# Optimization experiments

Measured on AMD Instinct MI355X. Metric: run time of the kernel, lower is better.

The kernel has to match this reference:

```python
import jax, jax.numpy as jnp
import numpy as np

N_NODES = 32
GAT_OUT = 64
LSTM_H = 128
N_CLS = 4
NEG_SLOPE = 0.2


def setup_inputs() -> dict:
    key = jax.random.key(0)
    ks = jax.random.split(key, 12)
    B, T, E = 32, 512, 96
    F, H = GAT_OUT, LSTM_H
    s = 0.05
    return {
        "x_seq": jax.random.normal(ks[0], (B, T, N_NODES), jnp.float32),
        "edge_index": jax.random.randint(ks[1], (2, E), 0, N_NODES, jnp.int32),
        # GATConv params (heads=1): lin weight [in=1, F], attention vectors [F], bias [F]
        "w_gat": jax.random.normal(ks[2], (1, F), jnp.float32) * s,
        "att_src": jax.random.normal(ks[3], (F,), jnp.float32) * s,
        "att_dst": jax.random.normal(ks[4], (F,), jnp.float32) * s,
        "b_gat": jnp.zeros((F,), jnp.float32),
        # LSTM params, torch gate order (i, f, g, o)
        "W_ih": jax.random.normal(ks[5], (N_NODES * F, 4 * H), jnp.float32) * s,
        "W_hh": jax.random.normal(ks[6], (H, 4 * H), jnp.float32) * s,
        "b_ih": jnp.zeros((4 * H,), jnp.float32),
        "b_hh": jnp.zeros((4 * H,), jnp.float32),
        # classifier
        "W_fc": jax.random.normal(ks[7], (H, N_CLS), jnp.float32) * s,
        "b_fc": jnp.zeros((N_CLS,), jnp.float32),
    }


def _forward(x_seq, edge_index, w_gat, att_src, att_dst, b_gat,
             W_ih, W_hh, b_ih, b_hh, W_fc, b_fc):
    B, T, N = x_seq.shape
    F = w_gat.shape[1]
    H = W_hh.shape[0]

    # --- GAT over all (B,T) steps at once (PyG GATConv, heads=1, self-loops) ---
    loops = jnp.arange(N, dtype=edge_index.dtype)
    src = jnp.concatenate([edge_index[0], loops])  # [Et]
    dst = jnp.concatenate([edge_index[1], loops])  # [Et]
    Et = src.shape[0]

    h = x_seq[..., None] * w_gat            # [B,T,N,F] (in_channels=1 linear)
    a_s = h @ att_src                        # [B,T,N]
    a_d = h @ att_dst                        # [B,T,N]
    e = a_s[..., src] + a_d[..., dst]        # [B,T,Et]
    e = jnp.where(e > 0, e, NEG_SLOPE * e)   # LeakyReLU(0.2)

    # segment softmax over destination node, batched over B*T
    e2 = jnp.moveaxis(e, -1, 0).reshape(Et, B * T)
    m = jax.ops.segment_max(e2, dst, num_segments=N)        # [N,B*T]
    ex = jnp.exp(e2 - m[dst])
    z = jax.ops.segment_sum(ex, dst, num_segments=N)        # [N,B*T]
    alpha = ex / z[dst]                                      # [Et,B*T]
    alpha = jnp.moveaxis(alpha.reshape(Et, B, T), 0, -1)     # [B,T,Et]

    msg = alpha[..., None] * h[:, :, src, :]                 # [B,T,Et,F]
    onehot = (dst[:, None] == jnp.arange(N)).astype(h.dtype)  # [Et,N]
    out = jnp.einsum('btef,en->btnf', msg, onehot) + b_gat    # [B,T,N,F]

    seq = out.reshape(B, T, N * F)           # [B,T,2048]

    # --- single-layer LSTM (batch_first), torch gate order i,f,g,o ---
    xw = seq @ W_ih + (b_ih + b_hh)          # [B,T,4H]

    def step(carry, xw_t):
        hs, cs = carry
        g = xw_t + hs @ W_hh                 # [B,4H]
        i, f, gg, o = jnp.split(g, 4, axis=-1)
        cs = jax.nn.sigmoid(f) * cs + jax.nn.sigmoid(i) * jnp.tanh(gg)
        hs = jax.nn.sigmoid(o) * jnp.tanh(cs)
        return (hs, cs), None

    h0 = jnp.zeros((B, H), seq.dtype)
    (h_last, _), _ = jax.lax.scan(step, (h0, h0), jnp.moveaxis(xw, 1, 0))

    return h_last @ W_fc + b_fc              # [B,num_classes]


def reference(x_seq, edge_index, w_gat, att_src, att_dst, b_gat,
              W_ih, W_hh, b_ih, b_hh, W_fc, b_fc):
    return _forward(x_seq, edge_index, w_gat, att_src, att_dst, b_gat,
                    W_ih, W_hh, b_ih, b_hh, W_fc, b_fc)
```

## Files before the change

### kernel.cpp

```cpp
#include <hip/hip_runtime.h>
#include <hip/hip_fp16.h>

#define NN 32
#define FF 64
#define HH 128
#define G4 512
#define BB 32
#define TT 512
#define ET 128
#define NPOS (BB*TT)
#define POSB 32

__device__ __forceinline__ float frcp(float x) { return __builtin_amdgcn_rcpf(x); }

__global__ __launch_bounds__(512) void prep_kernel(const float* __restrict__ w_gat,
                                                   const float* __restrict__ b_gat,
                                                   const float* __restrict__ W_ih,
                                                   const float* __restrict__ W_hh,
                                                   float* __restrict__ W_eff,
                                                   float* __restrict__ biasp,
                                                   float* __restrict__ Wt) {
  int j = threadIdx.x;
  int n = blockIdx.x;
  float accw = 0.f, accb = 0.f;
#pragma unroll 8
  for (int f = 0; f < FF; ++f) {
    float wv = W_ih[(n * FF + f) * G4 + j];
    accw = fmaf(w_gat[f], wv, accw);
    accb = fmaf(b_gat[f], wv, accb);
  }
  W_eff[n * G4 + j] = accw;
  biasp[n * G4 + j] = accb;
  __half* Wt16 = (__half*)Wt;
  int g0 = (n * G4 + j) * 4;
#pragma unroll
  for (int q = 0; q < 4; ++q) {
    int E = g0 + q;
    int tl = E >> 7, idx = E & 127;
    int r = tl >> 2, kq = tl & 3;
    int P = idx >> 3;
    int g = (idx >> 1) & 3;
    int e = idx & 1;
    int k = kq * 32 + 2 * P + e;
    Wt16[E] = __float2half(W_hh[k * G4 + g * 128 + r]);
  }
}

__global__ __launch_bounds__(256) void gatxw_kernel(const float* __restrict__ x_seq,
                                                    const int* __restrict__ ei,
                                                    const float* __restrict__ w_gat,
                                                    const float* __restrict__ att_src,
                                                    const float* __restrict__ att_dst,
                                                    const float* __restrict__ b_ih,
                                                    const float* __restrict__ b_hh,
                                                    const float* __restrict__ W_eff,
                                                    const float* __restrict__ biasp,
                                                    float* __restrict__ xw) {
  __shared__ int srt[ET];
  __shared__ int offs[NN + 1];
  __shared__ int cnt[NN];
  __shared__ float xs[POSB * NN];
  __shared__ float sl[POSB * NN];
  __shared__ float scal_sh[2];
  int tid = threadIdx.x;
  int posbase = blockIdx.x * POSB;
  float we0[NN], we1[NN];
#pragma unroll
  for (int nn = 0; nn < NN; ++nn) {
    we0[nn] = W_eff[nn * G4 + tid];
    we1[nn] = W_eff[nn * G4 + 256 + tid];
  }
  float b0 = b_ih[tid] + b_hh[tid];
  float b1 = b_ih[256 + tid] + b_hh[256 + tid];
#pragma unroll 8
  for (int n = 0; n < NN; ++n) {
    b0 += biasp[n * G4 + tid];
    b1 += biasp[n * G4 + 256 + tid];
  }
  if (tid < NN) cnt[tid] = 0;
  __syncthreads();
  int es = 0, ed = 0, tk = 0;
  if (tid < ET) {
    if (tid < 96) { es = ei[tid]; ed = ei[96 + tid]; }
    else { es = tid - 96; ed = tid - 96; }
    tk = atomicAdd(&cnt[ed], 1);
  }
  __syncthreads();
  if (tid == 0) {
    offs[0] = 0;
    for (int n = 0; n < NN; ++n) offs[n + 1] = offs[n] + cnt[n];
  }
  if (tid == 1) {
    float cs = 0.f, cd = 0.f;
    for (int f = 0; f < FF; ++f) {
      cs = fmaf(w_gat[f], att_src[f], cs);
      cd = fmaf(w_gat[f], att_dst[f], cd);
    }
    scal_sh[0] = cs;
    scal_sh[1] = cd;
  }
  __syncthreads();
  if (tid < ET) srt[offs[ed] + tk] = es;
#pragma unroll
  for (int c = 0; c < POSB * NN / 256; ++c)
    xs[c * 256 + tid] = x_seq[posbase * NN + c * 256 + tid];
  __syncthreads();
  float cs = scal_sh[0], cd = scal_sh[1];
  int n = tid & 31;
  int e0 = offs[n], e1 = offs[n + 1];
#pragma unroll
  for (int pb = 0; pb < POSB / 8; ++pb) {
    int p = pb * 8 + (tid >> 5);
    int base = p * 32;
    float xn = xs[base + n];
    float cdxn = cd * xn;
    float m = -3.0e38f;
    for (int e = e0; e < e1; ++e) {
      float ev = fmaf(cs, xs[base + srt[e]], cdxn);
      ev = ev > 0.f ? ev : 0.2f * ev;
      m = fmaxf(m, ev);
    }
    float z = 0.f, sa = 0.f;
    for (int e = e0; e < e1; ++e) {
      float xsv = xs[base + srt[e]];
      float ev = fmaf(cs, xsv, cdxn);
      ev = ev > 0.f ? ev : 0.2f * ev;
      float ex = __expf(ev - m);
      z += ex;
      sa = fmaf(ex, xsv, sa);
    }
    sl[base + n] = sa * frcp(z);
  }
  __syncthreads();
#pragma unroll 4
  for (int pp = 0; pp < POSB; ++pp) {
    const float4* sp = (const float4*)&sl[pp * 32];
    float a0 = b0, a1 = b1;
#pragma unroll
    for (int q = 0; q < 8; ++q) {
      float4 sv = sp[q];
      a0 = fmaf(sv.x, we0[4 * q], a0);
      a0 = fmaf(sv.y, we0[4 * q + 1], a0);
      a0 = fmaf(sv.z, we0[4 * q + 2], a0);
      a0 = fmaf(sv.w, we0[4 * q + 3], a0);
      a1 = fmaf(sv.x, we1[4 * q], a1);
      a1 = fmaf(sv.y, we1[4 * q + 1], a1);
      a1 = fmaf(sv.z, we1[4 * q + 2], a1);
      a1 = fmaf(sv.w, we1[4 * q + 3], a1);
    }
    size_t row = (size_t)(posbase + pp) * G4;
    xw[row + tid] = a0;
    xw[row + 256 + tid] = a1;
  }
}


#define D2F(HJ, W0, W1, W2, W3) \
  "v_dot2_f32_f16 v216, v" HJ ", v" W0 ", 0\n\t" \
  "v_dot2_f32_f16 v217, v" HJ ", v" W1 ", 0\n\t" \
  "v_dot2_f32_f16 v218, v" HJ ", v" W2 ", 0\n\t" \
  "v_dot2_f32_f16 v219, v" HJ ", v" W3 ", 0\n\t"

#define D2A(HJ, W0, W1, W2, W3) \
  "v_dot2_f32_f16 v216, v" HJ ", v" W0 ", v216\n\t" \
  "v_dot2_f32_f16 v217, v" HJ ", v" W1 ", v217\n\t" \
  "v_dot2_f32_f16 v218, v" HJ ", v" W2 ", v218\n\t" \
  "v_dot2_f32_f16 v219, v" HJ ", v" W3 ", v219\n\t"

#define PHASE(XSLOT, RD, WR) \
  "ds_read_b128 v[32:35], " RD "\n\t" \
  "ds_read_b128 v[36:39], " RD " offset:16\n\t" \
  "ds_read_b128 v[40:43], " RD " offset:32\n\t" \
  "ds_read_b128 v[44:47], " RD " offset:48\n\t" \
  "s_waitcnt lgkmcnt(3)\n\t" \
  D2F("32", "64", "65", "66", "67") \
  D2A("33", "68", "69", "70", "71") \
  D2A("34", "72", "73", "74", "75") \
  D2A("35", "76", "77", "78", "79") \
  "s_waitcnt lgkmcnt(2)\n\t" \
  D2A("36", "80", "81", "82", "83") \
  D2A("37", "84", "85", "86", "87") \
  D2A("38", "88", "89", "90", "91") \
  D2A("39", "92", "93", "94", "95") \
  "s_waitcnt lgkmcnt(1)\n\t" \
  D2A("40", "96", "97", "98", "99") \
  D2A("41", "100", "101", "102", "103") \
  D2A("42", "104", "105", "106", "107") \
  D2A("43", "108", "109", "110", "111") \
  "s_waitcnt lgkmcnt(0)\n\t" \
  D2A("44", "112", "113", "114", "115") \
  D2A("45", "116", "117", "118", "119") \
  D2A("46", "120", "121", "122", "123") \
  D2A("47", "124", "125", "126", "127") \
  "v_add_f32_dpp v216, v216, v216 quad_perm:[1,0,3,2] row_mask:0xf bank_mask:0xf\n\t" \
  "v_add_f32_dpp v217, v217, v217 quad_perm:[1,0,3,2] row_mask:0xf bank_mask:0xf\n\t" \
  "v_add_f32_dpp v218, v218, v218 quad_perm:[1,0,3,2] row_mask:0xf bank_mask:0xf\n\t" \
  "v_add_f32_dpp v219, v219, v219 quad_perm:[1,0,3,2] row_mask:0xf bank_mask:0xf\n\t" \
  "v_add_f32_dpp v216, v216, v216 quad_perm:[2,3,0,1] row_mask:0xf bank_mask:0xf\n\t" \
  "v_add_f32_dpp v217, v217, v217 quad_perm:[2,3,0,1] row_mask:0xf bank_mask:0xf\n\t" \
  "v_add_f32_dpp v218, v218, v218 quad_perm:[2,3,0,1] row_mask:0xf bank_mask:0xf\n\t" \
  "v_add_f32_dpp v219, v219, v219 quad_perm:[2,3,0,1] row_mask:0xf bank_mask:0xf\n\t" \
  "v_cndmask_b32 v208, v216, v217, s[22:23]\n\t" \
  "v_cndmask_b32 v209, v218, v219, s[22:23]\n\t" \
  "v_cndmask_b32 v208, v208, v209, s[24:25]\n\t" \
  "s_waitcnt vmcnt(3)\n\t" \
  "v_mov_b32 v215, " XSLOT "\n\t" \
  "global_load_dword " XSLOT ", v194, %[xwb]\n\t" \
  "v_add_u32 v194, 0x800, v194\n\t" \
  "v_add_f32 v208, v208, v215\n\t" \
  "v_mul_f32 v209, v200, v208\n\t" \
  "v_exp_f32 v209, v209\n\t" \
  "s_nop 0\n\t" \
  "v_add_f32 v209, 1.0, v209\n\t" \
  "v_rcp_f32 v209, v209\n\t" \
  "s_nop 0\n\t" \
  "v_fma_f32 v210, v201, v209, v202\n\t" \
  "s_nop 1\n\t" \
  "v_add_f32_dpp v211, v210, v203 quad_perm:[0,0,0,0] row_mask:0xf bank_mask:0xf\n\t" \
  "v_add_f32_dpp v212, v210, v203 quad_perm:[1,1,1,1] row_mask:0xf bank_mask:0xf\n\t" \
  "v_add_f32_dpp v213, v210, v203 quad_perm:[2,2,2,2] row_mask:0xf bank_mask:0xf\n\t" \
  "v_add_f32_dpp v214, v210, v203 quad_perm:[3,3,3,3] row_mask:0xf bank_mask:0xf\n\t" \
  "v_mul_f32 v211, v211, v213\n\t" \
  "v_fma_f32 v199, v212, v199, v211\n\t" \
  "v_mul_f32 v209, 0x4038aa3b, v199\n\t" \
  "v_exp_f32 v209, v209\n\t" \
  "s_nop 0\n\t" \
  "v_add_f32 v209, 1.0, v209\n\t" \
  "v_rcp_f32 v209, v209\n\t" \
  "s_nop 0\n\t" \
  "v_fma_f32 v209, -2.0, v209, 1.0\n\t" \
  "v_mul_f32 v209, v214, v209\n\t" \
  "v_cvt_f16_f32 v209, v209\n\t" \
  "ds_write_b16 " WR ", v209\n\t" \
  "s_waitcnt lgkmcnt(0)\n\t" \
  "s_barrier\n\t"

__global__ __launch_bounds__(512, 2) void lstm_kernel(const float* __restrict__ xw,
                                                      const float* __restrict__ Wt,
                                                      const float* __restrict__ W_fc,
                                                      const float* __restrict__ b_fc,
                                                      float* __restrict__ out) {
  __shared__ __align__(16) float lds[160];
  int b = blockIdx.x, tid = threadIdx.x;
  int r = tid >> 2, kq = tid & 3;
  if (tid < 160) lds[tid] = 0.f;
  const float* xwb = xw + (size_t)b * TT * G4;
  unsigned xoff0 = (unsigned)((kq * 128 + r) * 4);
  unsigned wtoff = (unsigned)(tid * 256);
  unsigned lbase = (unsigned)(uintptr_t)&lds[0];
  unsigned rda = lbase + (unsigned)(kq * 80);
  unsigned rdb = rda + 320;
  unsigned wra = lbase + (unsigned)(((r >> 5) * 40 + (r & 31)) * 2);
  unsigned wrb = wra + 320;
  float kmulf = (kq == 2) ? __uint_as_float(0x4038aa3bu)
                          : __uint_as_float(0xbfb8aa3bu);
  float Af = (kq == 2) ? -2.f : 1.f;
  float Bf = (kq == 2) ? 1.f : 0.f;
  unsigned kqodd = kq & 1, kqhi = kq >> 1;
  __syncthreads();
  asm volatile(
    "v_mov_b32 v194, %[xo]\n\t"
    "v_mov_b32 v195, %[rda]\n\t"
    "v_mov_b32 v196, %[rdb]\n\t"
    "v_mov_b32 v197, %[wra]\n\t"
    "v_mov_b32 v198, %[wrb]\n\t"
    "v_mov_b32 v199, 0\n\t"
    "v_mov_b32 v200, %[km]\n\t"
    "v_mov_b32 v201, %[Aa]\n\t"
    "v_mov_b32 v202, %[Bb]\n\t"
    "v_mov_b32 v203, 0\n\t"
    "v_cmp_eq_u32 s[22:23], 1, %[kodd]\n\t"
    "v_cmp_eq_u32 s[24:25], 1, %[khi]\n\t"
    "global_load_dword v224, v194, %[xwb]\n\t"
    "v_add_u32 v194, 0x800, v194\n\t"
    "global_load_dword v225, v194, %[xwb]\n\t"
    "v_add_u32 v194, 0x800, v194\n\t"
    "global_load_dword v226, v194, %[xwb]\n\t"
    "v_add_u32 v194, 0x800, v194\n\t"
    "global_load_dword v227, v194, %[xwb]\n\t"
    "v_add_u32 v194, 0x800, v194\n\t"
    "global_load_dwordx4 v[64:67], %[wto], %[wtb] offset:0\n\t"
    "global_load_dwordx4 v[68:71], %[wto], %[wtb] offset:16\n\t"
    "global_load_dwordx4 v[72:75], %[wto], %[wtb] offset:32\n\t"
    "global_load_dwordx4 v[76:79], %[wto], %[wtb] offset:48\n\t"
    "global_load_dwordx4 v[80:83], %[wto], %[wtb] offset:64\n\t"
    "global_load_dwordx4 v[84:87], %[wto], %[wtb] offset:80\n\t"
    "global_load_dwordx4 v[88:91], %[wto], %[wtb] offset:96\n\t"
    "global_load_dwordx4 v[92:95], %[wto], %[wtb] offset:112\n\t"
    "global_load_dwordx4 v[96:99], %[wto], %[wtb] offset:128\n\t"
    "global_load_dwordx4 v[100:103], %[wto], %[wtb] offset:144\n\t"
    "global_load_dwordx4 v[104:107], %[wto], %[wtb] offset:160\n\t"
    "global_load_dwordx4 v[108:111], %[wto], %[wtb] offset:176\n\t"
    "global_load_dwordx4 v[112:115], %[wto], %[wtb] offset:192\n\t"
    "global_load_dwordx4 v[116:119], %[wto], %[wtb] offset:208\n\t"
    "global_load_dwordx4 v[120:123], %[wto], %[wtb] offset:224\n\t"
    "global_load_dwordx4 v[124:127], %[wto], %[wtb] offset:240\n\t"
    "s_waitcnt vmcnt(0)\n\t"
    "s_movk_i32 s20, 0x80\n\t"
    "L_lstm_%=:\n\t"
    PHASE("v224", "v195", "v198")
    PHASE("v225", "v196", "v197")
    PHASE("v226", "v195", "v198")
    PHASE("v227", "v196", "v197")
    "s_sub_u32 s20, s20, 1\n\t"
    "s_cmp_lg_u32 s20, 0\n\t"
    "s_cbranch_scc1 L_lstm_%=\n\t"
    "s_waitcnt vmcnt(0) lgkmcnt(0)\n\t"
    :
    : [xwb]"s"(xwb), [wtb]"s"(Wt), [wto]"v"(wtoff), [xo]"v"(xoff0),
      [rda]"v"(rda), [rdb]"v"(rdb), [wra]"v"(wra), [wrb]"v"(wrb),
      [km]"v"(kmulf), [Aa]"v"(Af), [Bb]"v"(Bf),
      [kodd]"v"(kqodd), [khi]"v"(kqhi)
    : "memory", "scc", "s20", "s22", "s23", "s24", "s25",
      "v32","v33","v34","v35","v36","v37","v38","v39",
      "v40","v41","v42","v43","v44","v45","v46","v47",
      "v64","v65","v66","v67","v68","v69","v70","v71",
      "v72","v73","v74","v75","v76","v77","v78","v79",
      "v80","v81","v82","v83","v84","v85","v86","v87",
      "v88","v89","v90","v91","v92","v93","v94","v95",
      "v96","v97","v98","v99","v100","v101","v102","v103",
      "v104","v105","v106","v107","v108","v109","v110","v111",
      "v112","v113","v114","v115","v116","v117","v118","v119",
      "v120","v121","v122","v123","v124","v125","v126","v127",
      "v194","v195","v196","v197","v198","v199",
      "v200","v201","v202","v203","v204","v205","v206","v207",
      "v208","v209","v210","v211","v212","v213","v214","v215",
      "v216","v217","v218","v219",
      "v224","v225","v226","v227");
  __syncthreads();
  if (tid < 4) {
    const __half* hf = (const __half*)lds;
    float acc = b_fc[tid];
#pragma unroll 8
    for (int k = 0; k < HH; ++k)
      acc = fmaf(__half2float(hf[(k >> 5) * 40 + (k & 31)]), W_fc[k * 4 + tid], acc);
    out[b * 4 + tid] = acc;
  }
}

extern "C" void kernel_launch(void* const* d_in, const int* in_sizes, int n_in,
                              void* d_out, int out_size, void* d_ws, size_t ws_size,
                              hipStream_t stream) {
  const float* x_seq   = (const float*)d_in[0];
  const int*   ei      = (const int*)d_in[1];
  const float* w_gat   = (const float*)d_in[2];
  const float* att_src = (const float*)d_in[3];
  const float* att_dst = (const float*)d_in[4];
  const float* b_gat   = (const float*)d_in[5];
  const float* W_ih    = (const float*)d_in[6];
  const float* W_hh    = (const float*)d_in[7];
  const float* b_ih    = (const float*)d_in[8];
  const float* b_hh    = (const float*)d_in[9];
  const float* W_fc    = (const float*)d_in[10];
  const float* b_fc    = (const float*)d_in[11];

  float* ws = (float*)d_ws;
  float* Wt    = ws;
  float* xw    = Wt + 65536;
  float* W_eff = xw + (size_t)(NPOS + 8) * G4;
  float* biasp = W_eff + NN * G4;

  prep_kernel<<<NN, G4, 0, stream>>>(w_gat, b_gat, W_ih, W_hh, W_eff, biasp, Wt);
  gatxw_kernel<<<NPOS / POSB, 256, 0, stream>>>(x_seq, ei, w_gat, att_src, att_dst,
                                                b_ih, b_hh, W_eff, biasp, xw);
  lstm_kernel<<<BB, G4, 0, stream>>>(xw, Wt, W_fc, b_fc, (float*)d_out);
}
```

Measured before the change: 357.3 us.

## Fuse GAT and input projection into LSTM kernel, one block per batch

Merges the GAT attention and input-projection stage into the LSTM kernel. Each of the 32 blocks now computes the xw rows for its own batch element before running the recurrence, which removes one kernel launch and the grid-wide dependency between the two stages. The cost is that the GAT/projection work, which was spread over 512 blocks, now runs on only 32 blocks with 512 threads each. That serial prologue could take longer than the launch overhead it saves. xw still makes a round trip through global memory, guarded by a threadfence.

```diff
diff --git a/kernel.cpp b/kernel.cpp
--- a/kernel.cpp
+++ b/kernel.cpp
@@ -9,7 +9,6 @@
 #define TT 512
 #define ET 128
 #define NPOS (BB*TT)
-#define POSB 32
 
 __device__ __forceinline__ float frcp(float x) { return __builtin_amdgcn_rcpf(x); }
 
@@ -43,114 +42,6 @@
     int e = idx & 1;
     int k = kq * 32 + 2 * P + e;
     Wt16[E] = __float2half(W_hh[k * G4 + g * 128 + r]);
-  }
-}
-
-__global__ __launch_bounds__(256) void gatxw_kernel(const float* __restrict__ x_seq,
-                                                    const int* __restrict__ ei,
-                                                    const float* __restrict__ w_gat,
-                                                    const float* __restrict__ att_src,
-                                                    const float* __restrict__ att_dst,
-                                                    const float* __restrict__ b_ih,
-                                                    const float* __restrict__ b_hh,
-                                                    const float* __restrict__ W_eff,
-                                                    const float* __restrict__ biasp,
-                                                    float* __restrict__ xw) {
-  __shared__ int srt[ET];
-  __shared__ int offs[NN + 1];
-  __shared__ int cnt[NN];
-  __shared__ float xs[POSB * NN];
-  __shared__ float sl[POSB * NN];
-  __shared__ float scal_sh[2];
-  int tid = threadIdx.x;
-  int posbase = blockIdx.x * POSB;
-  float we0[NN], we1[NN];
-#pragma unroll
-  for (int nn = 0; nn < NN; ++nn) {
-    we0[nn] = W_eff[nn * G4 + tid];
-    we1[nn] = W_eff[nn * G4 + 256 + tid];
-  }
-  float b0 = b_ih[tid] + b_hh[tid];
-  float b1 = b_ih[256 + tid] + b_hh[256 + tid];
-#pragma unroll 8
-  for (int n = 0; n < NN; ++n) {
-    b0 += biasp[n * G4 + tid];
-    b1 += biasp[n * G4 + 256 + tid];
-  }
-  if (tid < NN) cnt[tid] = 0;
-  __syncthreads();
-  int es = 0, ed = 0, tk = 0;
-  if (tid < ET) {
-    if (tid < 96) { es = ei[tid]; ed = ei[96 + tid]; }
-    else { es = tid - 96; ed = tid - 96; }
-    tk = atomicAdd(&cnt[ed], 1);
-  }
-  __syncthreads();
-  if (tid == 0) {
-    offs[0] = 0;
-    for (int n = 0; n < NN; ++n) offs[n + 1] = offs[n] + cnt[n];
-  }
-  if (tid == 1) {
-    float cs = 0.f, cd = 0.f;
-    for (int f = 0; f < FF; ++f) {
-      cs = fmaf(w_gat[f], att_src[f], cs);
-      cd = fmaf(w_gat[f], att_dst[f], cd);
-    }
-    scal_sh[0] = cs;
-    scal_sh[1] = cd;
-  }
-  __syncthreads();
-  if (tid < ET) srt[offs[ed] + tk] = es;
-#pragma unroll
-  for (int c = 0; c < POSB * NN / 256; ++c)
-    xs[c * 256 + tid] = x_seq[posbase * NN + c * 256 + tid];
-  __syncthreads();
-  float cs = scal_sh[0], cd = scal_sh[1];
-  int n = tid & 31;
-  int e0 = offs[n], e1 = offs[n + 1];
-#pragma unroll
-  for (int pb = 0; pb < POSB / 8; ++pb) {
-    int p = pb * 8 + (tid >> 5);
-    int base = p * 32;
-    float xn = xs[base + n];
-    float cdxn = cd * xn;
-    float m = -3.0e38f;
-    for (int e = e0; e < e1; ++e) {
-      float ev = fmaf(cs, xs[base + srt[e]], cdxn);
-      ev = ev > 0.f ? ev : 0.2f * ev;
-      m = fmaxf(m, ev);
-    }
-    float z = 0.f, sa = 0.f;
-    for (int e = e0; e < e1; ++e) {
-      float xsv = xs[base + srt[e]];
-      float ev = fmaf(cs, xsv, cdxn);
-      ev = ev > 0.f ? ev : 0.2f * ev;
-      float ex = __expf(ev - m);
-      z += ex;
-      sa = fmaf(ex, xsv, sa);
-    }
-    sl[base + n] = sa * frcp(z);
-  }
-  __syncthreads();
-#pragma unroll 4
-  for (int pp = 0; pp < POSB; ++pp) {
-    const float4* sp = (const float4*)&sl[pp * 32];
-    float a0 = b0, a1 = b1;
-#pragma unroll
-    for (int q = 0; q < 8; ++q) {
-      float4 sv = sp[q];
-      a0 = fmaf(sv.x, we0[4 * q], a0);
-      a0 = fmaf(sv.y, we0[4 * q + 1], a0);
-      a0 = fmaf(sv.z, we0[4 * q + 2], a0);
-      a0 = fmaf(sv.w, we0[4 * q + 3], a0);
-      a1 = fmaf(sv.x, we1[4 * q], a1);
-      a1 = fmaf(sv.y, we1[4 * q + 1], a1);
-      a1 = fmaf(sv.z, we1[4 * q + 2], a1);
-      a1 = fmaf(sv.w, we1[4 * q + 3], a1);
-    }
-    size_t row = (size_t)(posbase + pp) * G4;
-    xw[row + tid] = a0;
-    xw[row + 256 + tid] = a1;
   }
 }
 
@@ -235,19 +126,118 @@
   "s_waitcnt lgkmcnt(0)\n\t" \
   "s_barrier\n\t"
 
-__global__ __launch_bounds__(512, 2) void lstm_kernel(const float* __restrict__ xw,
-                                                      const float* __restrict__ Wt,
-                                                      const float* __restrict__ W_fc,
-                                                      const float* __restrict__ b_fc,
-                                                      float* __restrict__ out) {
-  __shared__ __align__(16) float lds[160];
-  int b = blockIdx.x, tid = threadIdx.x;
+__global__ __launch_bounds__(512, 2) void fused_kernel(const float* __restrict__ x_seq,
+                                                       const int* __restrict__ ei,
+                                                       const float* __restrict__ w_gat,
+                                                       const float* __restrict__ att_src,
+                                                       const float* __restrict__ att_dst,
+                                                       const float* __restrict__ b_ih,
+                                                       const float* __restrict__ b_hh,
+                                                       const float* __restrict__ W_eff,
+                                                       const float* __restrict__ biasp,
+                                                       const float* __restrict__ Wt,
+                                                       const float* __restrict__ W_fc,
+                                                       const float* __restrict__ b_fc,
+                                                       float* __restrict__ xw,
+                                                       float* __restrict__ out) {
+  __shared__ int srt[ET];
+  __shared__ int offs[NN + 1];
+  __shared__ int cnt[NN];
+  __shared__ float xs[32 * NN];
+  __shared__ float sl[32 * NN];
+  __shared__ float scal_sh[2];
+  __shared__ __align__(16) float hlds[160];
+  int tid = threadIdx.x;
+  int b = blockIdx.x;
+  float* xwb_w = xw + (size_t)b * TT * G4;
+
+  float wcol[NN];
+#pragma unroll
+  for (int nn = 0; nn < NN; ++nn) wcol[nn] = W_eff[nn * G4 + tid];
+  float bcol = b_ih[tid] + b_hh[tid];
+#pragma unroll 8
+  for (int nn = 0; nn < NN; ++nn) bcol += biasp[nn * G4 + tid];
+  if (tid < NN) cnt[tid] = 0;
+  __syncthreads();
+  int es = 0, ed = 0, tk = 0;
+  if (tid < ET) {
+    if (tid < 96) { es = ei[tid]; ed = ei[96 + tid]; }
+    else { es = tid - 96; ed = tid - 96; }
+    tk = atomicAdd(&cnt[ed], 1);
+  }
+  __syncthreads();
+  if (tid == 0) {
+    offs[0] = 0;
+    for (int n = 0; n < NN; ++n) offs[n + 1] = offs[n] + cnt[n];
+  }
+  if (tid == 1) {
+    float cs = 0.f, cd = 0.f;
+    for (int f = 0; f < FF; ++f) {
+      cs = fmaf(w_gat[f], att_src[f], cs);
+      cd = fmaf(w_gat[f], att_dst[f], cd);
+    }
+    scal_sh[0] = cs;
+    scal_sh[1] = cd;
+  }
+  __syncthreads();
+  if (tid < ET) srt[offs[ed] + tk] = es;
+  __syncthreads();
+  int n = tid & 31;
+  int e0 = offs[n], e1 = offs[n + 1];
+  float cs = scal_sh[0], cd = scal_sh[1];
+  for (int rd = 0; rd < TT / 32; ++rd) {
+    size_t gbase = ((size_t)b * TT + rd * 32) * NN;
+    xs[tid] = x_seq[gbase + tid];
+    xs[512 + tid] = x_seq[gbase + 512 + tid];
+    __syncthreads();
+#pragma unroll
+    for (int pp2 = 0; pp2 < 2; ++pp2) {
+      int p = (tid >> 5) + pp2 * 16;
+      int base = p * 32;
+      float xn = xs[base + n];
+      float cdxn = cd * xn;
+      float m = -3.0e38f;
+      for (int e = e0; e < e1; ++e) {
+        float ev = fmaf(cs, xs[base + srt[e]], cdxn);
+        ev = ev > 0.f ? ev : 0.2f * ev;
+        m = fmaxf(m, ev);
+      }
+      float z = 0.f, sa = 0.f;
+      for (int e = e0; e < e1; ++e) {
+        float xsv = xs[base + srt[e]];
+        float ev = fmaf(cs, xsv, cdxn);
+        ev = ev > 0.f ? ev : 0.2f * ev;
+        float ex = __expf(ev - m);
+        z += ex;
+        sa = fmaf(ex, xsv, sa);
+      }
+      sl[base + n] = sa * frcp(z);
+    }
+    __syncthreads();
+#pragma unroll 4
+    for (int pp = 0; pp < 32; ++pp) {
+      const float4* sp = (const float4*)&sl[pp * 32];
+      float a0 = bcol;
+#pragma unroll
+      for (int q = 0; q < 8; ++q) {
+        float4 sv = sp[q];
+        a0 = fmaf(sv.x, wcol[4 * q], a0);
+        a0 = fmaf(sv.y, wcol[4 * q + 1], a0);
+        a0 = fmaf(sv.z, wcol[4 * q + 2], a0);
+        a0 = fmaf(sv.w, wcol[4 * q + 3], a0);
+      }
+      xwb_w[(size_t)(rd * 32 + pp) * G4 + tid] = a0;
+    }
+    __syncthreads();
+  }
+  __threadfence();
+
   int r = tid >> 2, kq = tid & 3;
-  if (tid < 160) lds[tid] = 0.f;
+  if (tid < 160) hlds[tid] = 0.f;
   const float* xwb = xw + (size_t)b * TT * G4;
   unsigned xoff0 = (unsigned)((kq * 128 + r) * 4);
   unsigned wtoff = (unsigned)(tid * 256);
-  unsigned lbase = (unsigned)(uintptr_t)&lds[0];
+  unsigned lbase = (unsigned)(uintptr_t)&hlds[0];
   unsigned rda = lbase + (unsigned)(kq * 80);
   unsigned rdb = rda + 320;
   unsigned wra = lbase + (unsigned)(((r >> 5) * 40 + (r & 31)) * 2);
@@ -329,7 +319,7 @@
       "v224","v225","v226","v227");
   __syncthreads();
   if (tid < 4) {
-    const __half* hf = (const __half*)lds;
+    const __half* hf = (const __half*)hlds;
     float acc = b_fc[tid];
 #pragma unroll 8
     for (int k = 0; k < HH; ++k)
@@ -361,7 +351,7 @@
   float* biasp = W_eff + NN * G4;
 
   prep_kernel<<<NN, G4, 0, stream>>>(w_gat, b_gat, W_ih, W_hh, W_eff, biasp, Wt);
-  gatxw_kernel<<<NPOS / POSB, 256, 0, stream>>>(x_seq, ei, w_gat, att_src, att_dst,
-                                                b_ih, b_hh, W_eff, biasp, xw);
-  lstm_kernel<<<BB, G4, 0, stream>>>(xw, Wt, W_fc, b_fc, (float*)d_out);
+  fused_kernel<<<BB, G4, 0, stream>>>(x_seq, ei, w_gat, att_src, att_dst,
+                                      b_ih, b_hh, W_eff, biasp, Wt, W_fc, b_fc,
+                                      xw, (float*)d_out);
 }
```

Result: slower. 508.2 us (+42.2%).

## Replace dot2 recurrent matvec with 16x16x32 MFMA and per-lane gate layout

Applied to the files above, without the earlier changes.

The LSTM recurrent product h@W_hh moves from v_dot2 with DPP cross-lane reductions onto v_mfma_f32_16x16x32_f16. W_hh is re-laid out so that each wave owns 16 hidden units across all four gates, and one lane ends up holding the i, f, g, o preactivations for its unit. This drops the DPP reduction, the cndmask selects and the gate shuffles, and removes the padded LDS layout for h. In exchange it adds MFMA latency, padded with s_nops, on the serial per-step critical path, and it issues four xw loads per step instead of one.

```diff
diff --git a/kernel.cpp b/kernel.cpp
--- a/kernel.cpp
+++ b/kernel.cpp
@@ -34,15 +34,17 @@
   __half* Wt16 = (__half*)Wt;
   int g0 = (n * G4 + j) * 4;
 #pragma unroll
-  for (int q = 0; q < 4; ++q) {
-    int E = g0 + q;
-    int tl = E >> 7, idx = E & 127;
-    int r = tl >> 2, kq = tl & 3;
-    int P = idx >> 3;
-    int g = (idx >> 1) & 3;
-    int e = idx & 1;
-    int k = kq * 32 + 2 * P + e;
-    Wt16[E] = __float2half(W_hh[k * G4 + g * 128 + r]);
+  for (int qq = 0; qq < 4; ++qq) {
+    int E = g0 + qq;
+    int tl = E >> 7;
+    int idx = E & 127;
+    int frag = idx >> 3;
+    int e = idx & 7;
+    int g = frag >> 2, q = frag & 3;
+    int w = tl >> 6, l = tl & 63;
+    int k = q * 32 + ((l >> 4) * 8) + e;
+    int col = g * 128 + w * 16 + (l & 15);
+    Wt16[E] = __float2half(W_hh[k * G4 + col]);
   }
 }
 
@@ -155,83 +157,66 @@
 }
 
 
-#define D2F(HJ, W0, W1, W2, W3) \
-  "v_dot2_f32_f16 v216, v" HJ ", v" W0 ", 0\n\t" \
-  "v_dot2_f32_f16 v217, v" HJ ", v" W1 ", 0\n\t" \
-  "v_dot2_f32_f16 v218, v" HJ ", v" W2 ", 0\n\t" \
-  "v_dot2_f32_f16 v219, v" HJ ", v" W3 ", 0\n\t"
-
-#define D2A(HJ, W0, W1, W2, W3) \
-  "v_dot2_f32_f16 v216, v" HJ ", v" W0 ", v216\n\t" \
-  "v_dot2_f32_f16 v217, v" HJ ", v" W1 ", v217\n\t" \
-  "v_dot2_f32_f16 v218, v" HJ ", v" W2 ", v218\n\t" \
-  "v_dot2_f32_f16 v219, v" HJ ", v" W3 ", v219\n\t"
-
-#define PHASE(XSLOT, RD, WR) \
+#define MFMA_Q(AQ, BI, BF, BG, BO) \
+  "v_mfma_f32_16x16x32_f16 v[216:219], v[" AQ "], v[" BI "], v[216:219]\n\t" \
+  "v_mfma_f32_16x16x32_f16 v[220:223], v[" AQ "], v[" BF "], v[220:223]\n\t" \
+  "v_mfma_f32_16x16x32_f16 v[224:227], v[" AQ "], v[" BG "], v[224:227]\n\t" \
+  "v_mfma_f32_16x16x32_f16 v[228:231], v[" AQ "], v[" BO "], v[228:231]\n\t"
+
+#define PHASE(X0, X1, X2, X3, RD, WR) \
+  "s_waitcnt vmcnt(4)\n\t" \
+  "v_mov_b32 v216, " X0 "\n\t" \
+  "v_mov_b32 v220, " X1 "\n\t" \
+  "v_mov_b32 v224, " X2 "\n\t" \
+  "v_mov_b32 v228, " X3 "\n\t" \
   "ds_read_b128 v[32:35], " RD "\n\t" \
-  "ds_read_b128 v[36:39], " RD " offset:16\n\t" \
-  "ds_read_b128 v[40:43], " RD " offset:32\n\t" \
-  "ds_read_b128 v[44:47], " RD " offset:48\n\t" \
+  "ds_read_b128 v[36:39], " RD " offset:64\n\t" \
+  "ds_read_b128 v[40:43], " RD " offset:128\n\t" \
+  "ds_read_b128 v[44:47], " RD " offset:192\n\t" \
   "s_waitcnt lgkmcnt(3)\n\t" \
-  D2F("32", "64", "65", "66", "67") \
-  D2A("33", "68", "69", "70", "71") \
-  D2A("34", "72", "73", "74", "75") \
-  D2A("35", "76", "77", "78", "79") \
+  MFMA_Q("32:35", "64:67",   "80:83",   "96:99",   "112:115") \
   "s_waitcnt lgkmcnt(2)\n\t" \
-  D2A("36", "80", "81", "82", "83") \
-  D2A("37", "84", "85", "86", "87") \
-  D2A("38", "88", "89", "90", "91") \
-  D2A("39", "92", "93", "94", "95") \
+  MFMA_Q("36:39", "68:71",   "84:87",   "100:103", "116:119") \
   "s_waitcnt lgkmcnt(1)\n\t" \
-  D2A("40", "96", "97", "98", "99") \
-  D2A("41", "100", "101", "102", "103") \
-  D2A("42", "104", "105", "106", "107") \
-  D2A("43", "108", "109", "110", "111") \
+  MFMA_Q("40:43", "72:75",   "88:91",   "104:107", "120:123") \
   "s_waitcnt lgkmcnt(0)\n\t" \
-  D2A("44", "112", "113", "114", "115") \
-  D2A("45", "116", "117", "118", "119") \
-  D2A("46", "120", "121", "122", "123") \
-  D2A("47", "124", "125", "126", "127") \
-  "v_add_f32_dpp v216, v216, v216 quad_perm:[1,0,3,2] row_mask:0xf bank_mask:0xf\n\t" \
-  "v_add_f32_dpp v217, v217, v217 quad_perm:[1,0,3,2] row_mask:0xf bank_mask:0xf\n\t" \
-  "v_add_f32_dpp v218, v218, v218 quad_perm:[1,0,3,2] row_mask:0xf bank_mask:0xf\n\t" \
-  "v_add_f32_dpp v219, v219, v219 quad_perm:[1,0,3,2] row_mask:0xf bank_mask:0xf\n\t" \
-  "v_add_f32_dpp v216, v216, v216 quad_perm:[2,3,0,1] row_mask:0xf bank_mask:0xf\n\t" \
-  "v_add_f32_dpp v217, v217, v217 quad_perm:[2,3,0,1] row_mask:0xf bank_mask:0xf\n\t" \
-  "v_add_f32_dpp v218, v218, v218 quad_perm:[2,3,0,1] row_mask:0xf bank_mask:0xf\n\t" \
-  "v_add_f32_dpp v219, v219, v219 quad_perm:[2,3,0,1] row_mask:0xf bank_mask:0xf\n\t" \
-  "v_cndmask_b32 v208, v216, v217, s[22:23]\n\t" \
-  "v_cndmask_b32 v209, v218, v219, s[22:23]\n\t" \
-  "v_cndmask_b32 v208, v208, v209, s[24:25]\n\t" \
-  "s_waitcnt vmcnt(3)\n\t" \
-  "v_mov_b32 v215, " XSLOT "\n\t" \
-  "global_load_dword " XSLOT ", v194, %[xwb]\n\t" \
+  MFMA_Q("44:47", "76:79",   "92:95",   "108:111", "124:127") \
+  "global_load_dword " X0 ", v194, %[xwb]\n\t" \
+  "global_load_dword " X1 ", v194, %[xwb] offset:512\n\t" \
+  "global_load_dword " X2 ", v194, %[xwb] offset:1024\n\t" \
+  "global_load_dword " X3 ", v194, %[xwb] offset:1536\n\t" \
   "v_add_u32 v194, 0x800, v194\n\t" \
-  "v_add_f32 v208, v208, v215\n\t" \
-  "v_mul_f32 v209, v200, v208\n\t" \
-  "v_exp_f32 v209, v209\n\t" \
+  "s_nop 7\n\t" \
+  "s_nop 7\n\t" \
+  "v_mul_f32 v204, v200, v216\n\t" \
+  "v_mul_f32 v205, v200, v220\n\t" \
+  "v_mul_f32 v206, v201, v224\n\t" \
+  "v_mul_f32 v207, v200, v228\n\t" \
+  "v_exp_f32 v204, v204\n\t" \
+  "v_exp_f32 v205, v205\n\t" \
+  "v_exp_f32 v206, v206\n\t" \
+  "v_exp_f32 v207, v207\n\t" \
+  "v_add_f32 v204, 1.0, v204\n\t" \
+  "v_add_f32 v205, 1.0, v205\n\t" \
+  "v_add_f32 v206, 1.0, v206\n\t" \
+  "v_add_f32 v207, 1.0, v207\n\t" \
+  "v_rcp_f32 v204, v204\n\t" \
+  "v_rcp_f32 v205, v205\n\t" \
+  "v_rcp_f32 v206, v206\n\t" \
+  "v_rcp_f32 v207, v207\n\t" \
+  "v_fma_f32 v206, -2.0, v206, 1.0\n\t" \
+  "v_mul_f32 v210, v204, v206\n\t" \
+  "v_fma_f32 v199, v205, v199, v210\n\t" \
+  "v_mul_f32 v211, v201, v199\n\t" \
+  "v_exp_f32 v211, v211\n\t" \
   "s_nop 0\n\t" \
-  "v_add_f32 v209, 1.0, v209\n\t" \
-  "v_rcp_f32 v209, v209\n\t" \
+  "v_add_f32 v211, 1.0, v211\n\t" \
+  "v_rcp_f32 v211, v211\n\t" \
   "s_nop 0\n\t" \
-  "v_fma_f32 v210, v201, v209, v202\n\t" \
-  "s_nop 1\n\t" \
-  "v_add_f32_dpp v211, v210, v203 quad_perm:[0,0,0,0] row_mask:0xf bank_mask:0xf\n\t" \
-  "v_add_f32_dpp v212, v210, v203 quad_perm:[1,1,1,1] row_mask:0xf bank_mask:0xf\n\t" \
-  "v_add_f32_dpp v213, v210, v203 quad_perm:[2,2,2,2] row_mask:0xf bank_mask:0xf\n\t" \
-  "v_add_f32_dpp v214, v210, v203 quad_perm:[3,3,3,3] row_mask:0xf bank_mask:0xf\n\t" \
-  "v_mul_f32 v211, v211, v213\n\t" \
-  "v_fma_f32 v199, v212, v199, v211\n\t" \
-  "v_mul_f32 v209, 0x4038aa3b, v199\n\t" \
-  "v_exp_f32 v209, v209\n\t" \
-  "s_nop 0\n\t" \
-  "v_add_f32 v209, 1.0, v209\n\t" \
-  "v_rcp_f32 v209, v209\n\t" \
-  "s_nop 0\n\t" \
-  "v_fma_f32 v209, -2.0, v209, 1.0\n\t" \
-  "v_mul_f32 v209, v214, v209\n\t" \
-  "v_cvt_f16_f32 v209, v209\n\t" \
-  "ds_write_b16 " WR ", v209\n\t" \
+  "v_fma_f32 v211, -2.0, v211, 1.0\n\t" \
+  "v_mul_f32 v211, v207, v211\n\t" \
+  "v_cvt_f16_f32 v211, v211\n\t" \
+  "ds_write_b16 " WR ", v211\n\t" \
   "s_waitcnt lgkmcnt(0)\n\t" \
   "s_barrier\n\t"
 
@@ -240,23 +225,19 @@
                                                       const float* __restrict__ W_fc,
                                                       const float* __restrict__ b_fc,
                                                       float* __restrict__ out) {
-  __shared__ __align__(16) float lds[160];
+  __shared__ __align__(16) float hlds[128];
   int b = blockIdx.x, tid = threadIdx.x;
-  int r = tid >> 2, kq = tid & 3;
-  if (tid < 160) lds[tid] = 0.f;
+  int w = tid >> 6, l = tid & 63;
+  int u = w * 16 + (l & 15);
+  if (tid < 128) hlds[tid] = 0.f;
   const float* xwb = xw + (size_t)b * TT * G4;
-  unsigned xoff0 = (unsigned)((kq * 128 + r) * 4);
+  unsigned xoff0 = (unsigned)(u * 4);
   unsigned wtoff = (unsigned)(tid * 256);
-  unsigned lbase = (unsigned)(uintptr_t)&lds[0];
-  unsigned rda = lbase + (unsigned)(kq * 80);
-  unsigned rdb = rda + 320;
-  unsigned wra = lbase + (unsigned)(((r >> 5) * 40 + (r & 31)) * 2);
-  unsigned wrb = wra + 320;
-  float kmulf = (kq == 2) ? __uint_as_float(0x4038aa3bu)
-                          : __uint_as_float(0xbfb8aa3bu);
-  float Af = (kq == 2) ? -2.f : 1.f;
-  float Bf = (kq == 2) ? 1.f : 0.f;
-  unsigned kqodd = kq & 1, kqhi = kq >> 1;
+  unsigned lbase = (unsigned)(uintptr_t)&hlds[0];
+  unsigned rda = lbase + (unsigned)((l >> 4) * 16);
+  unsigned rdb = rda + 256;
+  unsigned wra = lbase + (unsigned)(u * 2);
+  unsigned wrb = wra + 256;
   __syncthreads();
   asm volatile(
     "v_mov_b32 v194, %[xo]\n\t"
@@ -265,19 +246,21 @@
     "v_mov_b32 v197, %[wra]\n\t"
     "v_mov_b32 v198, %[wrb]\n\t"
     "v_mov_b32 v199, 0\n\t"
-    "v_mov_b32 v200, %[km]\n\t"
-    "v_mov_b32 v201, %[Aa]\n\t"
-    "v_mov_b32 v202, %[Bb]\n\t"
-    "v_mov_b32 v203, 0\n\t"
-    "v_cmp_eq_u32 s[22:23], 1, %[kodd]\n\t"
-    "v_cmp_eq_u32 s[24:25], 1, %[khi]\n\t"
-    "global_load_dword v224, v194, %[xwb]\n\t"
+    "v_mov_b32 v200, 0xbfb8aa3b\n\t"
+    "v_mov_b32 v201, 0x4038aa3b\n\t"
+    "v_mov_b32 v217, 0\n\t" "v_mov_b32 v218, 0\n\t" "v_mov_b32 v219, 0\n\t"
+    "v_mov_b32 v221, 0\n\t" "v_mov_b32 v222, 0\n\t" "v_mov_b32 v223, 0\n\t"
+    "v_mov_b32 v225, 0\n\t" "v_mov_b32 v226, 0\n\t" "v_mov_b32 v227, 0\n\t"
+    "v_mov_b32 v229, 0\n\t" "v_mov_b32 v230, 0\n\t" "v_mov_b32 v231, 0\n\t"
+    "global_load_dword v240, v194, %[xwb]\n\t"
+    "global_load_dword v241, v194, %[xwb] offset:512\n\t"
+    "global_load_dword v242, v194, %[xwb] offset:1024\n\t"
+    "global_load_dword v243, v194, %[xwb] offset:1536\n\t"
     "v_add_u32 v194, 0x800, v194\n\t"
-    "global_load_dword v225, v194, %[xwb]\n\t"
-    "v_add_u32 v194, 0x800, v194\n\t"
-    "global_load_dword v226, v194, %[xwb]\n\t"
-    "v_add_u32 v194, 0x800, v194\n\t"
-    "global_load_dword v227, v194, %[xwb]\n\t"
+    "global_load_dword v244, v194, %[xwb]\n\t"
+    "global_load_dword v245, v194, %[xwb] offset:512\n\t"
+    "global_load_dword v246, v194, %[xwb] offset:1024\n\t"
+    "global_load_dword v247, v194, %[xwb] offset:1536\n\t"
     "v_add_u32 v194, 0x800, v194\n\t"
     "global_load_dwordx4 v[64:67], %[wto], %[wtb] offset:0\n\t"
     "global_load_dwordx4 v[68:71], %[wto], %[wtb] offset:16\n\t"
@@ -296,22 +279,18 @@
     "global_load_dwordx4 v[120:123], %[wto], %[wtb] offset:224\n\t"
     "global_load_dwordx4 v[124:127], %[wto], %[wtb] offset:240\n\t"
     "s_waitcnt vmcnt(0)\n\t"
-    "s_movk_i32 s20, 0x80\n\t"
+    "s_movk_i32 s20, 0x100\n\t"
     "L_lstm_%=:\n\t"
-    PHASE("v224", "v195", "v198")
-    PHASE("v225", "v196", "v197")
-    PHASE("v226", "v195", "v198")
-    PHASE("v227", "v196", "v197")
+    PHASE("v240", "v241", "v242", "v243", "v195", "v198")
+    PHASE("v244", "v245", "v246", "v247", "v196", "v197")
     "s_sub_u32 s20, s20, 1\n\t"
     "s_cmp_lg_u32 s20, 0\n\t"
     "s_cbranch_scc1 L_lstm_%=\n\t"
     "s_waitcnt vmcnt(0) lgkmcnt(0)\n\t"
     :
     : [xwb]"s"(xwb), [wtb]"s"(Wt), [wto]"v"(wtoff), [xo]"v"(xoff0),
-      [rda]"v"(rda), [rdb]"v"(rdb), [wra]"v"(wra), [wrb]"v"(wrb),
-      [km]"v"(kmulf), [Aa]"v"(Af), [Bb]"v"(Bf),
-      [kodd]"v"(kqodd), [khi]"v"(kqhi)
-    : "memory", "scc", "s20", "s22", "s23", "s24", "s25",
+      [rda]"v"(rda), [rdb]"v"(rdb), [wra]"v"(wra), [wrb]"v"(wrb)
+    : "memory", "scc", "s20",
       "v32","v33","v34","v35","v36","v37","v38","v39",
       "v40","v41","v42","v43","v44","v45","v46","v47",
       "v64","v65","v66","v67","v68","v69","v70","v71",
@@ -322,18 +301,18 @@
       "v104","v105","v106","v107","v108","v109","v110","v111",
       "v112","v113","v114","v115","v116","v117","v118","v119",
       "v120","v121","v122","v123","v124","v125","v126","v127",
-      "v194","v195","v196","v197","v198","v199",
-      "v200","v201","v202","v203","v204","v205","v206","v207",
-      "v208","v209","v210","v211","v212","v213","v214","v215",
-      "v216","v217","v218","v219",
-      "v224","v225","v226","v227");
+      "v194","v195","v196","v197","v198","v199","v200","v201",
+      "v204","v205","v206","v207","v208","v209","v210","v211",
+      "v216","v217","v218","v219","v220","v221","v222","v223",
+      "v224","v225","v226","v227","v228","v229","v230","v231",
+      "v240","v241","v242","v243","v244","v245","v246","v247");
   __syncthreads();
   if (tid < 4) {
-    const __half* hf = (const __half*)lds;
+    const __half* hf = (const __half*)hlds;
     float acc = b_fc[tid];
 #pragma unroll 8
     for (int k = 0; k < HH; ++k)
-      acc = fmaf(__half2float(hf[(k >> 5) * 40 + (k & 31)]), W_fc[k * 4 + tid], acc);
+      acc = fmaf(__half2float(hf[k]), W_fc[k * 4 + tid], acc);
     out[b * 4 + tid] = acc;
   }
 }
```

New measurement: 335.8 us, median of 2. 1.06x faster.
